# Kernel tuning notes

Measured on AMD Instinct MI355X. Metric: run time of the kernel, lower is better.

Reference implementation:

```python
import jax, jax.numpy as jnp
import numpy as np

N_NODES = 50000
N_EDGES = 500000
D = 256  # node_dim = edge_dim = out_dim; in_dim = 2*D


def setup_inputs() -> dict:
    key = jax.random.key(0)
    ks = jax.random.split(key, 9)
    x = jax.random.normal(ks[0], (N_NODES, D), dtype=jnp.float32)
    edge_index = jax.random.randint(ks[1], (2, N_EDGES), 0, N_NODES, dtype=jnp.int64)
    edge_attr = jax.random.normal(ks[2], (N_EDGES, D), dtype=jnp.float32)
    u = jax.random.normal(ks[3], (1, D), dtype=jnp.float32)
    batch = jnp.zeros((N_NODES,), dtype=jnp.int64)
    scale = 1.0 / np.sqrt(2 * D)
    W1 = jax.random.normal(ks[4], (2 * D, D), dtype=jnp.float32) * scale
    b1 = jax.random.normal(ks[5], (D,), dtype=jnp.float32) * scale
    W2 = jax.random.normal(ks[6], (2 * D, D), dtype=jnp.float32) * scale
    b2 = jax.random.normal(ks[7], (D,), dtype=jnp.float32) * scale
    return {"x": x, "edge_index": edge_index, "edge_attr": edge_attr, "u": u,
            "batch": batch, "W1": W1, "b1": b1, "W2": W2, "b2": b2}


def reference(x, edge_index, edge_attr, u, batch, W1, b1, W2, b2):
    row, col = edge_index[0], edge_index[1]
    # gather source-node features and concat with edge features: [E, 2D]
    h = jnp.concatenate([x[row], edge_attr], axis=1)
    h = jax.nn.relu(h @ W1 + b1)  # node_mlp_1
    # scatter-mean over destination nodes
    agg = jax.ops.segment_sum(h, col, num_segments=N_NODES)
    cnt = jax.ops.segment_sum(jnp.ones((h.shape[0],), h.dtype), col, num_segments=N_NODES)
    agg = agg / jnp.maximum(cnt, 1.0)[:, None]
    out = jnp.concatenate([x, agg], axis=1)  # [N, 2D]
    return jax.nn.relu(out @ W2 + b2)  # node_mlp_2
```

## Files before the change

kernel.cpp:

```cpp
#include <hip/hip_runtime.h>

#define N_NODES 50000
#define N_EDGES 500000
#define D 256
#define TWO_D 512

typedef __attribute__((ext_vector_type(8))) __bf16 bf16x8;
typedef __attribute__((ext_vector_type(4))) float f32x4;
typedef unsigned short ushort_t;

__device__ __forceinline__ unsigned short f2bf(float f) {
    unsigned int u = __builtin_bit_cast(unsigned int, f);
    u += 0x7FFFu + ((u >> 16) & 1u);
    return (unsigned short)(u >> 16);
}
__device__ __forceinline__ unsigned int pk2(float lo, float hi) {
    return (unsigned int)f2bf(lo) | ((unsigned int)f2bf(hi) << 16);
}


__global__ void k_zero(float* __restrict__ p, int n4) {
    int i = blockIdx.x * blockDim.x + threadIdx.x;
    if (i < n4) ((float4*)p)[i] = make_float4(0.f, 0.f, 0.f, 0.f);
}

__global__ void k_cvt_x(const float* __restrict__ x, ushort_t* __restrict__ xb, int n8) {
    int i = blockIdx.x * blockDim.x + threadIdx.x;
    if (i < n8) {
        const float4* s = (const float4*)(x + (size_t)i * 8);
        float4 a = s[0], b = s[1];
        uint4 o;
        o.x = pk2(a.x, a.y); o.y = pk2(a.z, a.w);
        o.z = pk2(b.x, b.y); o.w = pk2(b.z, b.w);
        *(uint4*)(xb + (size_t)i * 8) = o;
    }
}

__global__ void k_wt(const float* __restrict__ w, ushort_t* __restrict__ wt, int KW) {
    int n = blockIdx.x;
    for (int k = threadIdx.x; k < KW; k += blockDim.x)
        wt[(size_t)n * KW + k] = f2bf(w[(size_t)k * D + n]);
}

__global__ void k_count_i(const int* __restrict__ coli, int* __restrict__ cnt) {
    int e = blockIdx.x * blockDim.x + threadIdx.x;
    if (e < N_EDGES) atomicAdd(&cnt[coli[e]], 1);
}


__device__ __forceinline__ int iscan_block(int v, int tid) {
    int lane = tid & 63, wv = tid >> 6;
    int s = v;
    #pragma unroll
    for (int off = 1; off < 64; off <<= 1) {
        int t = __shfl_up(s, off, 64);
        if (lane >= off) s += t;
    }
    __shared__ int wsum[4];
    if (lane == 63) wsum[wv] = s;
    __syncthreads();
    #pragma unroll
    for (int w = 0; w < 3; ++w)
        if (wv > w) s += wsum[w];
    return s;
}

__global__ void k_scan_a(const int* __restrict__ cnt, int* __restrict__ rowptr,
                         int* __restrict__ bsum) {
    int i = blockIdx.x * 256 + threadIdx.x;
    int v = (i < N_NODES) ? cnt[i] : 0;
    int s = iscan_block(v, threadIdx.x);
    if (i < N_NODES) rowptr[i] = s - v;
    if (threadIdx.x == 255) bsum[blockIdx.x] = s;
}

__global__ void k_scan_b(int* __restrict__ bsum, int nb) {
    int i = threadIdx.x;
    int v = (i < nb) ? bsum[i] : 0;
    int s = iscan_block(v, i);
    if (i < nb) bsum[i] = s - v;
}

__global__ void k_scan_c(int* __restrict__ rowptr, const int* __restrict__ bsum,
                         int* __restrict__ cursor) {
    int i = blockIdx.x * 256 + threadIdx.x;
    if (i < N_NODES) {
        int r = rowptr[i] + bsum[blockIdx.x];
        rowptr[i] = r;
        cursor[i] = r;
    }
    if (i == 0) rowptr[N_NODES] = N_EDGES;
}

__global__ void k_fill(const int* __restrict__ coli, const int* __restrict__ rowi,
                       int* __restrict__ cursor, int* __restrict__ elist,
                       int* __restrict__ rowg) {
    int e = blockIdx.x * blockDim.x + threadIdx.x;
    if (e < N_EDGES) {
        int p = atomicAdd(&cursor[coli[e]], 1);
        elist[p] = e;
        rowg[p] = rowi[e];
    }
}

__global__ void k_posnode(const int* __restrict__ rowptr, int* __restrict__ posnode) {
    int p = blockIdx.x * blockDim.x + threadIdx.x;
    if (p >= N_EDGES) return;
    int lo = 0, hi = N_NODES;
    while (hi - lo > 1) {
        int mid = (lo + hi) >> 1;
        if (rowptr[mid] <= p) lo = mid; else hi = mid;
    }
    posnode[p] = lo;
}

__global__ __launch_bounds__(256) void k_xw1(
    const ushort_t* __restrict__ xb, const ushort_t* __restrict__ w1at,
    const float* __restrict__ b1, float* __restrict__ xw1)
{
    __shared__ __align__(16) ushort_t As[64 * 64];
    __shared__ __align__(16) ushort_t Bs[256 * 64];
    const int tid = threadIdx.x;
    const int wave = tid >> 6, lane = tid & 63;
    const int lr = lane & 15, lh = lane >> 4;
    const int n0 = blockIdx.x * 64;

    const int sm = tid >> 2;
    const int sc = (tid & 3) << 4;
    int ns = n0 + sm; if (ns >= N_NODES) ns = N_NODES - 1;
    const ushort_t* xrow = xb + (size_t)ns * D;
    const ushort_t* wrow = w1at + (size_t)tid * D;
    const int swA = (sm & 7) << 3;
    const int swB = (tid & 7) << 3;

    f32x4 acc[4][4];
    #pragma unroll
    for (int i = 0; i < 4; ++i)
        #pragma unroll
        for (int j = 0; j < 4; ++j)
            acc[i][j] = (f32x4){0.f, 0.f, 0.f, 0.f};

    for (int kk = 0; kk < 4; ++kk) {
        const int k0 = kk << 6;
        const uint4* sx = (const uint4*)(xrow + k0 + sc);
        uint4 av0 = sx[0], av1 = sx[1];
        const uint4* wsv = (const uint4*)(wrow + k0);
        uint4 w0 = wsv[0], w1 = wsv[1], w2 = wsv[2], w3 = wsv[3];
        uint4 w4 = wsv[4], w5 = wsv[5], w6 = wsv[6], w7 = wsv[7];

        __syncthreads();
        *(uint4*)&As[sm * 64 + ( sc      ^ swA)] = av0;
        *(uint4*)&As[sm * 64 + ((sc + 8) ^ swA)] = av1;
        {
            const int base = tid * 64;
            *(uint4*)&Bs[base + ( 0 ^ swB)] = w0;
            *(uint4*)&Bs[base + ( 8 ^ swB)] = w1;
            *(uint4*)&Bs[base + (16 ^ swB)] = w2;
            *(uint4*)&Bs[base + (24 ^ swB)] = w3;
            *(uint4*)&Bs[base + (32 ^ swB)] = w4;
            *(uint4*)&Bs[base + (40 ^ swB)] = w5;
            *(uint4*)&Bs[base + (48 ^ swB)] = w6;
            *(uint4*)&Bs[base + (56 ^ swB)] = w7;
        }
        __syncthreads();

        #pragma unroll
        for (int kh = 0; kh < 2; ++kh) {
            const int kb = kh * 32 + lh * 8;
            bf16x8 af[4], bfr[4];
            #pragma unroll
            for (int i = 0; i < 4; ++i) {
                int m = i * 16 + lr;
                af[i] = *(const bf16x8*)&As[m * 64 + (kb ^ ((m & 7) << 3))];
            }
            #pragma unroll
            for (int j = 0; j < 4; ++j) {
                int n = wave * 64 + j * 16 + lr;
                bfr[j] = *(const bf16x8*)&Bs[n * 64 + (kb ^ ((n & 7) << 3))];
            }
            #pragma unroll
            for (int i = 0; i < 4; ++i)
                #pragma unroll
                for (int j = 0; j < 4; ++j)
                    acc[i][j] = __builtin_amdgcn_mfma_f32_16x16x32_bf16(af[i], bfr[j], acc[i][j], 0, 0, 0);
        }
    }

    float bv[4];
    #pragma unroll
    for (int j = 0; j < 4; ++j) bv[j] = b1[wave * 64 + j * 16 + lr];
    #pragma unroll
    for (int i = 0; i < 4; ++i) {
        #pragma unroll
        for (int r = 0; r < 4; ++r) {
            int m = i * 16 + lh * 4 + r;
            int node = n0 + m;
            if (node < N_NODES) {
                float* orow = xw1 + (size_t)node * D;
                #pragma unroll
                for (int j = 0; j < 4; ++j)
                    orow[wave * 64 + j * 16 + lr] = acc[i][j][r] + bv[j];
            }
        }
    }
}

__global__ __launch_bounds__(256) void k_edge_csr(
    const float* __restrict__ ea, const ushort_t* __restrict__ w1bt,
    const float* __restrict__ xw1, const int* __restrict__ elist,
    const int* __restrict__ rowg, const int* __restrict__ posnode,
    const int* __restrict__ rowptr, float* __restrict__ agg)
{
    __shared__ __align__(16) ushort_t As[64 * 64];
    __shared__ __align__(16) ushort_t Bs[256 * 64];
    __shared__ int snd[64];
    __shared__ int ssr[64];
    const int tid = threadIdx.x;
    const int wave = tid >> 6, lane = tid & 63;
    const int lr = lane & 15, lh = lane >> 4;
    const int p0 = blockIdx.x * 64;

    if (tid < 64) {
        int p = p0 + tid;
        int pc = min(p, N_EDGES - 1);
        snd[tid] = (p < N_EDGES) ? posnode[pc] : -1;
        ssr[tid] = rowg[pc];
    }

    const int sm = tid >> 2;
    const int sc = (tid & 3) << 4;
    int ps = p0 + sm; if (ps >= N_EDGES) ps = N_EDGES - 1;
    const int es = elist[ps];
    const float* earow = ea + (size_t)es * D;
    const ushort_t* wrow = w1bt + (size_t)tid * D;
    const int swA = (sm & 7) << 3;
    const int swB = (tid & 7) << 3;

    f32x4 acc[4][4];
    #pragma unroll
    for (int i = 0; i < 4; ++i)
        #pragma unroll
        for (int j = 0; j < 4; ++j)
            acc[i][j] = (f32x4){0.f, 0.f, 0.f, 0.f};

    #pragma unroll 1
    for (int kk = 0; kk < 4; ++kk) {
        const int k0 = kk << 6;
        const float4* s = (const float4*)(earow + k0 + sc);
        float4 f0 = s[0], f1 = s[1], f2 = s[2], f3 = s[3];
        uint4 av0, av1;
        av0.x = pk2(f0.x, f0.y); av0.y = pk2(f0.z, f0.w);
        av0.z = pk2(f1.x, f1.y); av0.w = pk2(f1.z, f1.w);
        av1.x = pk2(f2.x, f2.y); av1.y = pk2(f2.z, f2.w);
        av1.z = pk2(f3.x, f3.y); av1.w = pk2(f3.z, f3.w);
        const uint4* wsv = (const uint4*)(wrow + k0);
        uint4 w0 = wsv[0], w1 = wsv[1], w2 = wsv[2], w3 = wsv[3];
        uint4 w4 = wsv[4], w5 = wsv[5], w6 = wsv[6], w7 = wsv[7];

        __syncthreads();
        *(uint4*)&As[sm * 64 + ( sc      ^ swA)] = av0;
        *(uint4*)&As[sm * 64 + ((sc + 8) ^ swA)] = av1;
        {
            const int base = tid * 64;
            *(uint4*)&Bs[base + ( 0 ^ swB)] = w0;
            *(uint4*)&Bs[base + ( 8 ^ swB)] = w1;
            *(uint4*)&Bs[base + (16 ^ swB)] = w2;
            *(uint4*)&Bs[base + (24 ^ swB)] = w3;
            *(uint4*)&Bs[base + (32 ^ swB)] = w4;
            *(uint4*)&Bs[base + (40 ^ swB)] = w5;
            *(uint4*)&Bs[base + (48 ^ swB)] = w6;
            *(uint4*)&Bs[base + (56 ^ swB)] = w7;
        }
        __syncthreads();

        #pragma unroll
        for (int kh = 0; kh < 2; ++kh) {
            const int kb = kh * 32 + lh * 8;
            bf16x8 af[4], bfr[4];
            #pragma unroll
            for (int i = 0; i < 4; ++i) {
                int m = i * 16 + lr;
                af[i] = *(const bf16x8*)&As[m * 64 + (kb ^ ((m & 7) << 3))];
            }
            #pragma unroll
            for (int j = 0; j < 4; ++j) {
                int n = wave * 64 + j * 16 + lr;
                bfr[j] = *(const bf16x8*)&Bs[n * 64 + (kb ^ ((n & 7) << 3))];
            }
            #pragma unroll
            for (int i = 0; i < 4; ++i)
                #pragma unroll
                for (int j = 0; j < 4; ++j)
                    acc[i][j] = __builtin_amdgcn_mfma_f32_16x16x32_bf16(af[i], bfr[j], acc[i][j], 0, 0, 0);
        }
    }

    #pragma unroll
    for (int i = 0; i < 4; ++i) {
        #pragma unroll
        for (int r = 0; r < 4; ++r) {
            const int m = i * 16 + lh * 4 + r;
            const bool ok = (p0 + m < N_EDGES);
            const int srow = ssr[m];
            const float* xr = xw1 + (size_t)srow * D + wave * 64 + lr;
            #pragma unroll
            for (int j = 0; j < 4; ++j) {
                float v = acc[i][j][r] + xr[j * 16];
                v = v > 0.f ? v : 0.f;
                acc[i][j][r] = ok ? v : 0.f;
            }
        }
    }

    int a = 0;
    while (a < 64) {
        const int node = snd[a];
        int b = a + 1;
        while (b < 64 && snd[b] == node) ++b;
        if (node >= 0) {
            float s0 = 0.f, s1 = 0.f, s2 = 0.f, s3 = 0.f;
            #pragma unroll
            for (int i = 0; i < 4; ++i) {
                if (b <= i * 16 || a >= (i + 1) * 16) continue;
                #pragma unroll
                for (int r = 0; r < 4; ++r) {
                    const int m = i * 16 + lh * 4 + r;
                    const bool in = (m >= a) && (m < b);
                    s0 += in ? acc[i][0][r] : 0.f;
                    s1 += in ? acc[i][1][r] : 0.f;
                    s2 += in ? acc[i][2][r] : 0.f;
                    s3 += in ? acc[i][3][r] : 0.f;
                }
            }
            s0 += __shfl_xor(s0, 16, 64); s0 += __shfl_xor(s0, 32, 64);
            s1 += __shfl_xor(s1, 16, 64); s1 += __shfl_xor(s1, 32, 64);
            s2 += __shfl_xor(s2, 16, 64); s2 += __shfl_xor(s2, 32, 64);
            s3 += __shfl_xor(s3, 16, 64); s3 += __shfl_xor(s3, 32, 64);
            if (lh == 0) {
                const bool interior = (rowptr[node] >= p0) && (rowptr[node + 1] <= p0 + 64);
                float* dst = agg + (size_t)node * D + wave * 64 + lr;
                if (interior) {
                    dst[0]  = s0; dst[16] = s1; dst[32] = s2; dst[48] = s3;
                } else {
                    atomicAdd(&dst[0],  s0); atomicAdd(&dst[16], s1);
                    atomicAdd(&dst[32], s2); atomicAdd(&dst[48], s3);
                }
            }
        }
        a = b;
    }
}

__global__ __launch_bounds__(256) void k_node(
    const ushort_t* __restrict__ xb, const float* __restrict__ agg,
    const int* __restrict__ cnti,
    const ushort_t* __restrict__ w2t, const float* __restrict__ b2,
    float* __restrict__ out)
{
    __shared__ __align__(16) ushort_t As[64 * 64];
    __shared__ __align__(16) ushort_t Bs[256 * 64];
    const int tid = threadIdx.x;
    const int wave = tid >> 6, lane = tid & 63;
    const int lr = lane & 15, lh = lane >> 4;
    const int n0 = blockIdx.x * 64;

    const int sm = tid >> 2;
    const int sc = (tid & 3) << 4;
    int ns = n0 + sm; if (ns >= N_NODES) ns = N_NODES - 1;
    const ushort_t* xrow = xb + (size_t)ns * D;
    const float*    arow = agg + (size_t)ns * D;
    const float     ic   = 1.0f / fmaxf((float)cnti[ns], 1.0f);
    const ushort_t* wrow = w2t + (size_t)tid * TWO_D;
    const int swA = (sm & 7) << 3;
    const int swB = (tid & 7) << 3;

    f32x4 acc[4][4];
    #pragma unroll
    for (int i = 0; i < 4; ++i)
        #pragma unroll
        for (int j = 0; j < 4; ++j)
            acc[i][j] = (f32x4){0.f, 0.f, 0.f, 0.f};

    for (int kk = 0; kk < 8; ++kk) {
        const int k0 = kk << 6;
        uint4 av0, av1;
        if (kk < 4) {
            const uint4* s = (const uint4*)(xrow + k0 + sc);
            av0 = s[0]; av1 = s[1];
        } else {
            const float4* s = (const float4*)(arow + (k0 - D) + sc);
            float4 f0 = s[0], f1 = s[1], f2 = s[2], f3 = s[3];
            f0.x *= ic; f0.y *= ic; f0.z *= ic; f0.w *= ic;
            f1.x *= ic; f1.y *= ic; f1.z *= ic; f1.w *= ic;
            f2.x *= ic; f2.y *= ic; f2.z *= ic; f2.w *= ic;
            f3.x *= ic; f3.y *= ic; f3.z *= ic; f3.w *= ic;
            av0.x = pk2(f0.x, f0.y); av0.y = pk2(f0.z, f0.w);
            av0.z = pk2(f1.x, f1.y); av0.w = pk2(f1.z, f1.w);
            av1.x = pk2(f2.x, f2.y); av1.y = pk2(f2.z, f2.w);
            av1.z = pk2(f3.x, f3.y); av1.w = pk2(f3.z, f3.w);
        }
        const uint4* wsv = (const uint4*)(wrow + k0);
        uint4 w0 = wsv[0], w1 = wsv[1], w2 = wsv[2], w3 = wsv[3];
        uint4 w4 = wsv[4], w5 = wsv[5], w6 = wsv[6], w7 = wsv[7];

        __syncthreads();
        *(uint4*)&As[sm * 64 + ( sc      ^ swA)] = av0;
        *(uint4*)&As[sm * 64 + ((sc + 8) ^ swA)] = av1;
        {
            const int base = tid * 64;
            *(uint4*)&Bs[base + ( 0 ^ swB)] = w0;
            *(uint4*)&Bs[base + ( 8 ^ swB)] = w1;
            *(uint4*)&Bs[base + (16 ^ swB)] = w2;
            *(uint4*)&Bs[base + (24 ^ swB)] = w3;
            *(uint4*)&Bs[base + (32 ^ swB)] = w4;
            *(uint4*)&Bs[base + (40 ^ swB)] = w5;
            *(uint4*)&Bs[base + (48 ^ swB)] = w6;
            *(uint4*)&Bs[base + (56 ^ swB)] = w7;
        }
        __syncthreads();

        #pragma unroll
        for (int kh = 0; kh < 2; ++kh) {
            const int kb = kh * 32 + lh * 8;
            bf16x8 af[4], bfr[4];
            #pragma unroll
            for (int i = 0; i < 4; ++i) {
                int m = i * 16 + lr;
                af[i] = *(const bf16x8*)&As[m * 64 + (kb ^ ((m & 7) << 3))];
            }
            #pragma unroll
            for (int j = 0; j < 4; ++j) {
                int n = wave * 64 + j * 16 + lr;
                bfr[j] = *(const bf16x8*)&Bs[n * 64 + (kb ^ ((n & 7) << 3))];
            }
            #pragma unroll
            for (int i = 0; i < 4; ++i)
                #pragma unroll
                for (int j = 0; j < 4; ++j)
                    acc[i][j] = __builtin_amdgcn_mfma_f32_16x16x32_bf16(af[i], bfr[j], acc[i][j], 0, 0, 0);
        }
    }

    float bv[4];
    #pragma unroll
    for (int j = 0; j < 4; ++j) bv[j] = b2[wave * 64 + j * 16 + lr];
    #pragma unroll
    for (int i = 0; i < 4; ++i) {
        #pragma unroll
        for (int r = 0; r < 4; ++r) {
            int m = i * 16 + lh * 4 + r;
            int node = n0 + m;
            if (node < N_NODES) {
                float* orow = out + (size_t)node * D;
                #pragma unroll
                for (int j = 0; j < 4; ++j) {
                    float v = acc[i][j][r] + bv[j];
                    orow[wave * 64 + j * 16 + lr] = v > 0.f ? v : 0.f;
                }
            }
        }
    }
}


extern "C" void kernel_launch(void* const* d_in, const int* in_sizes, int n_in,
                              void* d_out, int out_size, void* d_ws, size_t ws_size,
                              hipStream_t stream)
{
    const float* x  = (const float*)d_in[0];
    const int*   ei = (const int*)d_in[1];
    const float* ea = (const float*)d_in[2];
    const float* W1 = (const float*)d_in[5];
    const float* b1 = (const float*)d_in[6];
    const float* W2 = (const float*)d_in[7];
    const float* b2 = (const float*)d_in[8];
    float* out = (float*)d_out;

    const int* rowi = ei;
    const int* coli = ei + N_EDGES;
    char* ws = (char*)d_ws;

    size_t off = 0;
    auto take = [&](size_t bytes) {
        char* p = ws + off;
        off = (off + bytes + 255) & ~(size_t)255;
        return p;
    };

    ushort_t* xb      = (ushort_t*)take((size_t)N_NODES * D * 2);
    ushort_t* w1at    = (ushort_t*)take((size_t)D * D * 2);
    ushort_t* w1bt    = (ushort_t*)take((size_t)D * D * 2);
    ushort_t* w2t     = (ushort_t*)take((size_t)D * TWO_D * 2);
    float*    xw1     = (float*)take((size_t)N_NODES * D * 4);
    float*    agg     = (float*)take((size_t)N_NODES * D * 4);
    int*      cnti    = (int*)take(50016 * 4);
    int*      rowptr  = (int*)take(50016 * 4);
    int*      cursor  = (int*)take(50016 * 4);
    int*      bsum    = (int*)take(256 * 4);
    int*      elist   = (int*)take((size_t)N_EDGES * 4);
    int*      rowg    = (int*)take((size_t)N_EDGES * 4);
    int*      posnode = (int*)take((size_t)N_EDGES * 4);

    const int NB = (N_NODES + 255) / 256;
    const int EB = (N_EDGES + 255) / 256;
    const int NGB = (N_NODES + 63) / 64;
    const int EGB = (N_EDGES + 63) / 64;

    k_cvt_x<<<(N_NODES * D / 8 + 255) / 256, 256, 0, stream>>>(x, xb, N_NODES * D / 8);
    k_wt   <<<D, 256, 0, stream>>>(W1, w1at, D);
    k_wt   <<<D, 256, 0, stream>>>(W1 + (size_t)D * D, w1bt, D);
    k_wt   <<<D, 256, 0, stream>>>(W2, w2t, TWO_D);

    k_zero   <<<49, 256, 0, stream>>>((float*)cnti, 50016 / 4);
    k_count_i<<<EB, 256, 0, stream>>>(coli, cnti);
    k_scan_a <<<NB, 256, 0, stream>>>(cnti, rowptr, bsum);
    k_scan_b <<<1, 256, 0, stream>>>(bsum, NB);
    k_scan_c <<<NB, 256, 0, stream>>>(rowptr, bsum, cursor);
    k_fill   <<<EB, 256, 0, stream>>>(coli, rowi, cursor, elist, rowg);
    k_posnode<<<EB, 256, 0, stream>>>(rowptr, posnode);

    k_xw1    <<<NGB, 256, 0, stream>>>(xb, w1at, b1, xw1);
    k_zero   <<<(N_NODES * D / 4 + 255) / 256, 256, 0, stream>>>(agg, N_NODES * D / 4);
    k_edge_csr<<<EGB, 256, 0, stream>>>(ea, w1bt, xw1, elist, rowg, posnode, rowptr, agg);
    k_node   <<<NGB, 256, 0, stream>>>(xb, agg, cnti, w2t, b2, out);
}
```

Before: 546.5 us.

## Shrink edge-GEMM K tile to 32 with padded LDS rows for higher occupancy

The edge kernel's K step drops from 64 to 32, doubling the loop count. LDS tiles switch from XOR-swizzled 64-wide rows to padded 40-wide rows, which cuts shared memory per block. A launch bound of 3 blocks per SM is added, and the per-edge source-row indices are read straight from global memory in the epilogue instead of being staged in LDS. The aim is more resident blocks to hide gather latency, at the cost of twice as many barriers and possible LDS bank conflicts from the padded layout.

```diff
diff --git a/kernel.cpp b/kernel.cpp
--- a/kernel.cpp
+++ b/kernel.cpp
@@ -205,16 +205,15 @@
     }
 }
 
-__global__ __launch_bounds__(256) void k_edge_csr(
+__global__ __launch_bounds__(256, 3) void k_edge_csr(
     const float* __restrict__ ea, const ushort_t* __restrict__ w1bt,
     const float* __restrict__ xw1, const int* __restrict__ elist,
     const int* __restrict__ rowg, const int* __restrict__ posnode,
     const int* __restrict__ rowptr, float* __restrict__ agg)
 {
-    __shared__ __align__(16) ushort_t As[64 * 64];
-    __shared__ __align__(16) ushort_t Bs[256 * 64];
+    __shared__ __align__(16) ushort_t As[64 * 40];
+    __shared__ __align__(16) ushort_t Bs[256 * 40];
     __shared__ int snd[64];
-    __shared__ int ssr[64];
     const int tid = threadIdx.x;
     const int wave = tid >> 6, lane = tid & 63;
     const int lr = lane & 15, lh = lane >> 4;
@@ -222,19 +221,15 @@
 
     if (tid < 64) {
         int p = p0 + tid;
-        int pc = min(p, N_EDGES - 1);
-        snd[tid] = (p < N_EDGES) ? posnode[pc] : -1;
-        ssr[tid] = rowg[pc];
+        snd[tid] = (p < N_EDGES) ? posnode[min(p, N_EDGES - 1)] : -1;
     }
 
     const int sm = tid >> 2;
-    const int sc = (tid & 3) << 4;
+    const int scq = (tid & 3) << 3;
     int ps = p0 + sm; if (ps >= N_EDGES) ps = N_EDGES - 1;
     const int es = elist[ps];
     const float* earow = ea + (size_t)es * D;
     const ushort_t* wrow = w1bt + (size_t)tid * D;
-    const int swA = (sm & 7) << 3;
-    const int swB = (tid & 7) << 3;
 
     f32x4 acc[4][4];
     #pragma unroll
@@ -244,49 +239,36 @@
             acc[i][j] = (f32x4){0.f, 0.f, 0.f, 0.f};
 
     #pragma unroll 1
-    for (int kk = 0; kk < 4; ++kk) {
-        const int k0 = kk << 6;
-        const float4* s = (const float4*)(earow + k0 + sc);
-        float4 f0 = s[0], f1 = s[1], f2 = s[2], f3 = s[3];
-        uint4 av0, av1;
-        av0.x = pk2(f0.x, f0.y); av0.y = pk2(f0.z, f0.w);
-        av0.z = pk2(f1.x, f1.y); av0.w = pk2(f1.z, f1.w);
-        av1.x = pk2(f2.x, f2.y); av1.y = pk2(f2.z, f2.w);
-        av1.z = pk2(f3.x, f3.y); av1.w = pk2(f3.z, f3.w);
-        const uint4* wsv = (const uint4*)(wrow + k0);
-        uint4 w0 = wsv[0], w1 = wsv[1], w2 = wsv[2], w3 = wsv[3];
-        uint4 w4 = wsv[4], w5 = wsv[5], w6 = wsv[6], w7 = wsv[7];
+    for (int kk = 0; kk < 8; ++kk) {
+        const int k0 = kk << 5;
+        const float4* s = (const float4*)(earow + k0 + scq);
+        float4 f0 = s[0], f1 = s[1];
+        uint4 av;
+        av.x = pk2(f0.x, f0.y); av.y = pk2(f0.z, f0.w);
+        av.z = pk2(f1.x, f1.y); av.w = pk2(f1.z, f1.w);
+        const uint4* w = (const uint4*)(wrow + k0);
+        uint4 w0 = w[0], w1 = w[1], w2 = w[2], w3 = w[3];
 
         __syncthreads();
-        *(uint4*)&As[sm * 64 + ( sc      ^ swA)] = av0;
-        *(uint4*)&As[sm * 64 + ((sc + 8) ^ swA)] = av1;
+        *(uint4*)&As[sm * 40 + scq] = av;
         {
-            const int base = tid * 64;
-            *(uint4*)&Bs[base + ( 0 ^ swB)] = w0;
-            *(uint4*)&Bs[base + ( 8 ^ swB)] = w1;
-            *(uint4*)&Bs[base + (16 ^ swB)] = w2;
-            *(uint4*)&Bs[base + (24 ^ swB)] = w3;
-            *(uint4*)&Bs[base + (32 ^ swB)] = w4;
-            *(uint4*)&Bs[base + (40 ^ swB)] = w5;
-            *(uint4*)&Bs[base + (48 ^ swB)] = w6;
-            *(uint4*)&Bs[base + (56 ^ swB)] = w7;
+            ushort_t* bb = &Bs[tid * 40];
+            *(uint4*)&bb[ 0] = w0;
+            *(uint4*)&bb[ 8] = w1;
+            *(uint4*)&bb[16] = w2;
+            *(uint4*)&bb[24] = w3;
         }
         __syncthreads();
 
-        #pragma unroll
-        for (int kh = 0; kh < 2; ++kh) {
-            const int kb = kh * 32 + lh * 8;
+        {
+            const int kb = lh * 8;
             bf16x8 af[4], bfr[4];
             #pragma unroll
-            for (int i = 0; i < 4; ++i) {
-                int m = i * 16 + lr;
-                af[i] = *(const bf16x8*)&As[m * 64 + (kb ^ ((m & 7) << 3))];
-            }
-            #pragma unroll
-            for (int j = 0; j < 4; ++j) {
-                int n = wave * 64 + j * 16 + lr;
-                bfr[j] = *(const bf16x8*)&Bs[n * 64 + (kb ^ ((n & 7) << 3))];
-            }
+            for (int i = 0; i < 4; ++i)
+                af[i] = *(const bf16x8*)&As[(i * 16 + lr) * 40 + kb];
+            #pragma unroll
+            for (int j = 0; j < 4; ++j)
+                bfr[j] = *(const bf16x8*)&Bs[(wave * 64 + j * 16 + lr) * 40 + kb];
             #pragma unroll
             for (int i = 0; i < 4; ++i)
                 #pragma unroll
@@ -301,8 +283,8 @@
         for (int r = 0; r < 4; ++r) {
             const int m = i * 16 + lh * 4 + r;
             const bool ok = (p0 + m < N_EDGES);
-            const int srow = ssr[m];
-            const float* xr = xw1 + (size_t)srow * D + wave * 64 + lr;
+            const int srw = rowg[min(p0 + m, N_EDGES - 1)];
+            const float* xr = xw1 + (size_t)srw * D + wave * 64 + lr;
             #pragma unroll
             for (int j = 0; j < 4; ++j) {
                 float v = acc[i][j][r] + xr[j * 16];
```

Result: faster. 502.4 us (-8.1%).
